# Optimization experiments

Hardware: AMD Instinct MI355X
Metric: run time of the kernel (lower is better)

Reference implementation:

```python
import jax, jax.numpy as jnp
import numpy as np

SEQ, EMB, OUT = 8192, 1024, 128

def setup_inputs() -> dict:
    key = jax.random.key(0)
    k1, k2, k3, k4 = jax.random.split(key, 4)
    return {
        "x": jax.random.normal(k1, (SEQ, EMB), dtype=jnp.float32),
        "wquery": jax.random.normal(k2, (EMB, OUT), dtype=jnp.float32) * (2.0 / EMB) ** 0.5,
        "wkey": jax.random.normal(k3, (EMB, OUT), dtype=jnp.float32) * (2.0 / EMB) ** 0.5,
        "wvalue": jax.random.normal(k4, (EMB, OUT), dtype=jnp.float32) * (2.0 / EMB) ** 0.5,
    }

def reference(x, wquery, wkey, wvalue):
    # Single-head attention, mask=True branch (mask tensor is zeros -> no masking).
    q = x @ wquery   # [S, D]
    k = x @ wkey     # [S, D]
    v = x @ wvalue   # [S, D]
    scale = jnp.sqrt(jnp.asarray(q.shape[-1], dtype=q.dtype))
    a = (q @ k.T) / scale              # [S, S]
    p = jax.nn.softmax(a, axis=1)      # softmax over keys (dim=1 in torch)
    return p @ v                       # [S, D]
```

## Files before the change

kernel.cpp:

```cpp
#include <hip/hip_runtime.h>
#include <cstdint>
#include <cstddef>

#define SEQ 8192
#define EMB 1024
#define DH  128

typedef __bf16 bf16x8 __attribute__((ext_vector_type(8)));
typedef __bf16 bf16x2 __attribute__((ext_vector_type(2)));
typedef float  f32x4  __attribute__((ext_vector_type(4)));
typedef float  f32x16 __attribute__((ext_vector_type(16)));
typedef uint32_t u32x4 __attribute__((ext_vector_type(4)));
typedef unsigned short u16x8 __attribute__((ext_vector_type(8)));

static constexpr float QSCALE = (float)(1.4426950408889634 / 11.313708498984760);

__device__ __forceinline__ unsigned short f2bf(float f) {
  uint32_t u = __builtin_bit_cast(uint32_t, f);
  u += 0x7FFFu + ((u >> 16) & 1u);
  return (unsigned short)(u >> 16);
}
__device__ __forceinline__ float bf2f(unsigned short u) {
  return __builtin_bit_cast(float, (uint32_t)u << 16);
}

#define GLD_LDS16(gsrc, ldst) \
  __builtin_amdgcn_global_load_lds((__attribute__((address_space(1))) void*)(gsrc), \
                                   (__attribute__((address_space(3))) void*)(ldst), 16, 0, 0)

__global__ __launch_bounds__(256) void convert_kernel(
    const float* __restrict__ wq, const float* __restrict__ wk, const float* __restrict__ wv,
    unsigned short* __restrict__ wt)
{
  const int bid = blockIdx.x;
  const int t = threadIdx.x;
  const int which = bid >> 2;
  const int k = (bid & 3) * 256 + t;
  const float* w = (which == 0) ? wq : ((which == 1) ? wk : wv);
  const float scl = (which == 0) ? QSCALE : 1.0f;
#pragma unroll
  for (int n = 0; n < 128; n += 4) {
    float4 v = *reinterpret_cast<const float4*>(w + (size_t)k * DH + n);
    wt[((size_t)which * DH + n + 0) * EMB + k] = f2bf(v.x * scl);
    wt[((size_t)which * DH + n + 1) * EMB + k] = f2bf(v.y * scl);
    wt[((size_t)which * DH + n + 2) * EMB + k] = f2bf(v.z * scl);
    wt[((size_t)which * DH + n + 3) * EMB + k] = f2bf(v.w * scl);
  }
}

__global__ __launch_bounds__(256) void qkv_gemm(
    const float* __restrict__ x, const unsigned short* __restrict__ wt,
    unsigned short* __restrict__ qs, unsigned short* __restrict__ ks,
    unsigned short* __restrict__ vt)
{
  __shared__ char LDS[49152];
  char* A0 = LDS;
  char* B0 = LDS + 16384;
  unsigned short* T = (unsigned short*)LDS;

  const int t    = threadIdx.x;
  const int lane = t & 63;
  const int wid  = t >> 6;
  const int wr   = wid >> 1, wc = wid & 1;
  const int l31  = lane & 31;
  const int hi   = lane >> 5;
  const int row0 = blockIdx.x * 64;
  const int which = blockIdx.y;

  const char* wtc = (const char*)(wt + (size_t)which * DH * EMB);

  const int arow = t >> 2;
  const int aq   = t & 3;
  const float* xrow = x + (size_t)(row0 + arow) * EMB + aq * 16;
  const int awz = (arow & 7) << 4;
  const int aoff0 = (aq * 32 + 0)  ^ awz;
  const int aoff1 = (aq * 32 + 16) ^ awz;

  f32x16 acc[2] = {};
  float4 xa0, xa1, xa2, xa3;

  auto ALOAD = [&](int k0) {
    const float* s = xrow + k0;
    xa0 = *reinterpret_cast<const float4*>(s + 0);
    xa1 = *reinterpret_cast<const float4*>(s + 4);
    xa2 = *reinterpret_cast<const float4*>(s + 8);
    xa3 = *reinterpret_cast<const float4*>(s + 12);
  };
  auto AWRITE = [&](int buf) {
    bf16x8 h0 = { (__bf16)xa0.x, (__bf16)xa0.y, (__bf16)xa0.z, (__bf16)xa0.w,
                  (__bf16)xa1.x, (__bf16)xa1.y, (__bf16)xa1.z, (__bf16)xa1.w };
    bf16x8 h1 = { (__bf16)xa2.x, (__bf16)xa2.y, (__bf16)xa2.z, (__bf16)xa2.w,
                  (__bf16)xa3.x, (__bf16)xa3.y, (__bf16)xa3.z, (__bf16)xa3.w };
    char* base = A0 + buf * 8192 + arow * 128;
    *reinterpret_cast<bf16x8*>(base + aoff0) = h0;
    *reinterpret_cast<bf16x8*>(base + aoff1) = h1;
  };
  auto BSTAGE = [&](int buf, int k0) {
#pragma unroll
    for (int i = 0; i < 4; ++i) {
      int bidx = i * 4096 + t * 16;
      int n = bidx >> 7, off = bidx & 127;
      const char* src = wtc + (size_t)n * (EMB * 2) + k0 * 2 + (off ^ ((n & 7) << 4));
      GLD_LDS16(src, B0 + buf * 16384 + i * 4096 + wid * 1024);
    }
  };

  constexpr int NI = EMB / 64;

  ALOAD(0);
  BSTAGE(0, 0);
  AWRITE(0);
  ALOAD(64);
  asm volatile("s_waitcnt vmcnt(4) lgkmcnt(0)" ::: "memory");
  __builtin_amdgcn_s_barrier();
  asm volatile("" ::: "memory");

  for (int it = 0; it < NI; ++it) {
    const int cur = it & 1;
    if (it + 1 < NI) BSTAGE(cur ^ 1, (it + 1) * 64);

    const char* Ab = A0 + cur * 8192;
    const char* Bb = B0 + cur * 16384;
    const int ar   = wr * 32 + l31;
    const int aswz = (l31 & 7) << 4;

    __builtin_amdgcn_s_setprio(1);
#pragma unroll
    for (int kk = 0; kk < 4; ++kk) {
      bf16x8 af = *reinterpret_cast<const bf16x8*>(Ab + ar * 128 + ((kk * 32 + hi * 16) ^ aswz));
#pragma unroll
      for (int nt = 0; nt < 2; ++nt) {
        const int n = wc * 64 + nt * 32 + l31;
        bf16x8 bf = *reinterpret_cast<const bf16x8*>(Bb + n * 128 + ((kk * 32 + hi * 16) ^ ((n & 7) << 4)));
        acc[nt] = __builtin_amdgcn_mfma_f32_32x32x16_bf16(af, bf, acc[nt], 0, 0, 0);
      }
    }
    __builtin_amdgcn_s_setprio(0);

    if (it + 1 < NI) {
      AWRITE(cur ^ 1);
      if (it + 2 < NI) {
        ALOAD((it + 2) * 64);
        asm volatile("s_waitcnt vmcnt(4) lgkmcnt(0)" ::: "memory");
      } else {
        asm volatile("s_waitcnt vmcnt(0) lgkmcnt(0)" ::: "memory");
      }
    }
    __builtin_amdgcn_s_barrier();
    asm volatile("" ::: "memory");
  }

  if (which < 2) {
    unsigned short* dst = (which == 0) ? qs : ks;
#pragma unroll
    for (int nt = 0; nt < 2; ++nt)
#pragma unroll
      for (int r = 0; r < 16; ++r) {
        int row = row0 + wr * 32 + (r & 3) + 8 * (r >> 2) + 4 * hi;
        dst[(size_t)row * DH + wc * 64 + nt * 32 + l31] = f2bf(acc[nt][r]);
      }
  } else {
    __syncthreads();
#pragma unroll
    for (int nt = 0; nt < 2; ++nt)
#pragma unroll
      for (int r = 0; r < 16; ++r) {
        int d  = wc * 64 + nt * 32 + l31;
        int rl = wr * 32 + (r & 3) + 8 * (r >> 2) + 4 * hi;
        T[d * 72 + rl] = f2bf(acc[nt][r]);
      }
    __syncthreads();
    const int d = t >> 1, half = t & 1;
#pragma unroll
    for (int i = 0; i < 4; ++i) {
      uint4 v = *reinterpret_cast<const uint4*>(&T[d * 72 + half * 32 + i * 8]);
      *reinterpret_cast<uint4*>(vt + (size_t)d * SEQ + row0 + half * 32 + i * 8) = v;
    }
  }
}

template <int NS>
__global__ __launch_bounds__(512, 2) void attn_kernel(
    const unsigned short* __restrict__ qs, const unsigned short* __restrict__ ks,
    const unsigned short* __restrict__ vt,
    unsigned short* __restrict__ Obf, float* __restrict__ ml)
{
  __shared__ unsigned short Ks[2][64 * 128];
  __shared__ unsigned short Vt[2][128 * 64];

  const int t    = threadIdx.x;
  const int lane = t & 63;
  const int wid  = t >> 6;
  const int l31  = lane & 31;
  const int hi   = lane >> 5;
  const int kswz = (l31 & 15) << 4;
  const int q0   = blockIdx.x * 256 + wid * 32;
  const int sp   = blockIdx.y;

  bf16x8 qf[8];
  {
    const unsigned short* qp = qs + (size_t)(q0 + l31) * DH + hi * 8;
#pragma unroll
    for (int ds = 0; ds < 8; ++ds)
      qf[ds] = *reinterpret_cast<const bf16x8*>(qp + ds * 16);
  }

  float l = 0.f;
  f32x16 O[4] = {};

  const char* ksc = (const char*)ks;
  const char* vtc = (const char*)vt;
  char* ksl = (char*)&Ks[0][0];
  char* vtl = (char*)&Vt[0][0];

  constexpr int CHUNK = SEQ / NS;
  constexpr int NT = CHUNK / 64;
  const int kv_base = sp * CHUNK;

  auto KSTAGE = [&](int tile) {
    const int kv0 = kv_base + tile * 64;
#pragma unroll
    for (int rr = 0; rr < 2; ++rr) {
      int bidx = rr * 512 + t;
      int key = bidx >> 4, blk = bidx & 15;
      const char* src = ksc + (size_t)(kv0 + key) * 256 + ((blk * 16) ^ ((key & 15) << 4));
      GLD_LDS16(src, ksl + (tile & 1) * 16384 + rr * 8192 + wid * 1024);
    }
  };
  auto VSTAGE = [&](int tile) {
    const int kv0 = kv_base + tile * 64;
#pragma unroll
    for (int rr = 0; rr < 2; ++rr) {
      int bidx = rr * 512 + t;
      int rowi = bidx >> 4, ci = bidx & 15;
      int s = ci ^ (rowi & 15);
      int d = rowi * 2 + (s >> 3);
      int kb = s & 7;
      const char* src = vtc + (size_t)d * (SEQ * 2) + (size_t)kv0 * 2 + kb * 16;
      GLD_LDS16(src, vtl + (tile & 1) * 16384 + rr * 8192 + wid * 1024);
    }
  };

  auto QKT = [&](f32x16& T0, f32x16& T1, int tile) {
    const char* kb = ksl + (tile & 1) * 16384;
    f32x16 z = {};
    T0 = z; T1 = z;
#pragma unroll
    for (int ds = 0; ds < 8; ++ds) {
      bf16x8 ka = *reinterpret_cast<const bf16x8*>(kb + l31 * 256 + ((ds * 32 + hi * 16) ^ kswz));
      T0 = __builtin_amdgcn_mfma_f32_32x32x16_bf16(ka, qf[ds], T0, 0, 0, 0);
    }
#pragma unroll
    for (int ds = 0; ds < 8; ++ds) {
      bf16x8 ka = *reinterpret_cast<const bf16x8*>(kb + 8192 + l31 * 256 + ((ds * 32 + hi * 16) ^ kswz));
      T1 = __builtin_amdgcn_mfma_f32_32x32x16_bf16(ka, qf[ds], T1, 0, 0, 0);
    }
  };

  auto build2 = [&](const f32x16& P, bf16x8* fr) {
    uint32_t c[8];
#pragma unroll
    for (int i = 0; i < 8; ++i) {
      bf16x2 b2; b2[0] = (__bf16)P[2 * i]; b2[1] = (__bf16)P[2 * i + 1];
      c[i] = __builtin_bit_cast(uint32_t, b2);
    }
    uint32_t r0 = __shfl_xor(c[0], 32, 64), r1 = __shfl_xor(c[1], 32, 64);
    uint32_t r2 = __shfl_xor(c[2], 32, 64), r3 = __shfl_xor(c[3], 32, 64);
    u32x4 w0;
    w0[0] = hi ? r2 : c[0];
    w0[1] = hi ? r3 : c[1];
    w0[2] = hi ? c[2] : r0;
    w0[3] = hi ? c[3] : r1;
    uint32_t r4 = __shfl_xor(c[4], 32, 64), r5 = __shfl_xor(c[5], 32, 64);
    uint32_t r6 = __shfl_xor(c[6], 32, 64), r7 = __shfl_xor(c[7], 32, 64);
    u32x4 w1;
    w1[0] = hi ? r6 : c[4];
    w1[1] = hi ? r7 : c[5];
    w1[2] = hi ? c[6] : r4;
    w1[3] = hi ? c[7] : r5;
    fr[0] = __builtin_bit_cast(bf16x8, w0);
    fr[1] = __builtin_bit_cast(bf16x8, w1);
  };

  auto BODY = [&](int it, f32x16& Sc0, f32x16& Sc1, f32x16& Sn0, f32x16& Sn1) {
    if (it + 2 < NT) KSTAGE(it + 2);
    if (it + 1 < NT) VSTAGE(it + 1);

    if (it + 1 < NT) {
      __builtin_amdgcn_s_setprio(1);
      QKT(Sn0, Sn1, it + 1);
      __builtin_amdgcn_s_setprio(0);
    }

    float sm[16];
#pragma unroll
    for (int r = 0; r < 16; ++r) {
      Sc0[r] = __builtin_amdgcn_exp2f(Sc0[r]);
      Sc1[r] = __builtin_amdgcn_exp2f(Sc1[r]);
      sm[r] = Sc0[r] + Sc1[r];
    }
#pragma unroll
    for (int st = 8; st >= 1; st >>= 1)
#pragma unroll
      for (int r = 0; r < st; ++r) sm[r] += sm[r + st];
    l += sm[0] + __shfl_xor(sm[0], 32, 64);

    bf16x8 pa[4];
    build2(Sc0, &pa[0]);
    build2(Sc1, &pa[2]);

    const char* vb0 = vtl + (it & 1) * 16384;
    __builtin_amdgcn_s_setprio(1);
#pragma unroll
    for (int ks4 = 0; ks4 < 4; ++ks4) {
#pragma unroll
      for (int nt = 0; nt < 4; ++nt) {
        const int d = nt * 32 + l31;
        const int vrow = d >> 1;
        const int within = (((d & 1) << 3) | (ks4 * 2 + hi)) ^ (vrow & 15);
        bf16x8 vb = *reinterpret_cast<const bf16x8*>(vb0 + vrow * 256 + within * 16);
        O[nt] = __builtin_amdgcn_mfma_f32_32x32x16_bf16(pa[ks4], vb, O[nt], 0, 0, 0);
      }
    }
    __builtin_amdgcn_s_setprio(0);

    asm volatile("s_waitcnt vmcnt(0)" ::: "memory");
    __builtin_amdgcn_s_barrier();
    asm volatile("" ::: "memory");
  };

  KSTAGE(0); VSTAGE(0); KSTAGE(1);
  asm volatile("s_waitcnt vmcnt(0)" ::: "memory");
  __builtin_amdgcn_s_barrier();
  asm volatile("" ::: "memory");

  f32x16 Sa0, Sa1, Sb0, Sb1;
  QKT(Sa0, Sa1, 0);
  asm volatile("" ::: "memory");
  __builtin_amdgcn_s_barrier();
  asm volatile("" ::: "memory");

  for (int it = 0; it < NT; it += 2) {
    BODY(it,     Sa0, Sa1, Sb0, Sb1);
    BODY(it + 1, Sb0, Sb1, Sa0, Sa1);
  }

  const float linv = 1.0f / l;
  unsigned short* Obase = Obf + ((size_t)sp * SEQ + q0) * DH;
#pragma unroll
  for (int r = 0; r < 16; ++r) {
    const int row = (r & 3) + 8 * (r >> 2) + 4 * hi;
    const float li = __shfl(linv, row, 64);
#pragma unroll
    for (int nt = 0; nt < 4; ++nt)
      Obase[(size_t)row * DH + nt * 32 + l31] = f2bf(O[nt][r] * li);
  }
  if (lane < 32) {
    ml[(size_t)sp * (2 * SEQ) + q0 + lane]       = 0.0f;
    ml[(size_t)sp * (2 * SEQ) + SEQ + q0 + lane] = l;
  }
}

template <int NS>
__global__ __launch_bounds__(256) void combine_kernel(
    const unsigned short* __restrict__ Obf, const float* __restrict__ ml, float* __restrict__ out)
{
  const int idx = blockIdx.x * 256 + threadIdx.x;
  const int s = idx >> 4;
  const int c = (idx & 15) * 8;
  float mv[NS], lv[NS];
  float M = -__builtin_inff();
#pragma unroll
  for (int i = 0; i < NS; ++i) {
    mv[i] = ml[(size_t)i * (2 * SEQ) + s];
    lv[i] = ml[(size_t)i * (2 * SEQ) + SEQ + s];
    M = fmaxf(M, mv[i]);
  }
  float den = 0.f;
  float num[8] = {};
#pragma unroll
  for (int i = 0; i < NS; ++i) {
    float g = __builtin_amdgcn_exp2f(mv[i] - M) * lv[i];
    den += g;
    u16x8 o = *reinterpret_cast<const u16x8*>(&Obf[((size_t)i * SEQ + s) * DH + c]);
#pragma unroll
    for (int j = 0; j < 8; ++j) num[j] += g * bf2f(o[j]);
  }
  const float inv = 1.f / den;
  f32x4 r0, r1;
#pragma unroll
  for (int j = 0; j < 4; ++j) { r0[j] = num[j] * inv; r1[j] = num[j + 4] * inv; }
  *reinterpret_cast<f32x4*>(&out[(size_t)s * DH + c])     = r0;
  *reinterpret_cast<f32x4*>(&out[(size_t)s * DH + c + 4]) = r1;
}

extern "C" void kernel_launch(void* const* d_in, const int* in_sizes, int n_in,
                              void* d_out, int out_size, void* d_ws, size_t ws_size,
                              hipStream_t stream) {
  const float* x  = (const float*)d_in[0];
  const float* wq = (const float*)d_in[1];
  const float* wk = (const float*)d_in[2];
  const float* wv = (const float*)d_in[3];
  float* out = (float*)d_out;

  char* ws = (char*)d_ws;
  const size_t MB = 1024 * 1024;
  unsigned short* qs = (unsigned short*)(ws);
  unsigned short* ks = (unsigned short*)(ws + 2 * MB);
  unsigned short* vt = (unsigned short*)(ws + 4 * MB);
  unsigned short* wt = (unsigned short*)(ws + 6 * MB);

  convert_kernel<<<12, 256, 0, stream>>>(wq, wk, wv, wt);
  qkv_gemm<<<dim3(SEQ / 64, 3), 256, 0, stream>>>(x, wt, qs, ks, vt);

  unsigned short* Obf = (unsigned short*)(ws + 6 * MB);
  const size_t need8 = 6 * MB + 8ull * SEQ * DH * 2 + 8ull * 2 * SEQ * 4;
  if (ws_size >= need8) {
    float* ml = (float*)(ws + 6 * MB + 8ull * SEQ * DH * 2);
    attn_kernel<8><<<dim3(SEQ / 256, 8), 512, 0, stream>>>(qs, ks, vt, Obf, ml);
    combine_kernel<8><<<SEQ * DH / 8 / 256, 256, 0, stream>>>(Obf, ml, out);
  } else {
    float* ml = (float*)(ws + 6 * MB + 4ull * SEQ * DH * 2);
    attn_kernel<4><<<dim3(SEQ / 256, 4), 512, 0, stream>>>(qs, ks, vt, Obf, ml);
    combine_kernel<4><<<SEQ * DH / 8 / 256, 256, 0, stream>>>(Obf, ml, out);
  }
}
```

Before: 78.29 us.

## Double QKV GEMM block to 512 threads with one 32x32 tile per wave

The QKV projection GEMM now runs 8 waves per block instead of 4, so each wave computes a single 32x32 MFMA tile rather than two. The LDS layout of A and B changes to a paired-row XOR swizzle so that each thread stages one 16-byte chunk per load. The aim is more waves in flight to hide global-load latency in this memory-heavy stage. The cost is fewer MFMAs per barrier and more synchronisation per unit of work.

```diff
diff --git a/kernel.cpp b/kernel.cpp
--- a/kernel.cpp
+++ b/kernel.cpp
@@ -48,7 +48,7 @@
   }
 }
 
-__global__ __launch_bounds__(256) void qkv_gemm(
+__global__ __launch_bounds__(512) void qkv_gemm(
     const float* __restrict__ x, const unsigned short* __restrict__ wt,
     unsigned short* __restrict__ qs, unsigned short* __restrict__ ks,
     unsigned short* __restrict__ vt)
@@ -61,7 +61,8 @@
   const int t    = threadIdx.x;
   const int lane = t & 63;
   const int wid  = t >> 6;
-  const int wr   = wid >> 1, wc = wid & 1;
+  const int wr   = wid >> 2;
+  const int wc   = wid & 3;
   const int l31  = lane & 31;
   const int hi   = lane >> 5;
   const int row0 = blockIdx.x * 64;
@@ -69,39 +70,34 @@
 
   const char* wtc = (const char*)(wt + (size_t)which * DH * EMB);
 
-  const int arow = t >> 2;
-  const int aq   = t & 3;
-  const float* xrow = x + (size_t)(row0 + arow) * EMB + aq * 16;
-  const int awz = (arow & 7) << 4;
-  const int aoff0 = (aq * 32 + 0)  ^ awz;
-  const int aoff1 = (aq * 32 + 16) ^ awz;
-
-  f32x16 acc[2] = {};
-  float4 xa0, xa1, xa2, xa3;
+  const int arow = t >> 3;
+  const int ac8  = t & 7;
+  const float* xrow = x + (size_t)(row0 + arow) * EMB + ac8 * 8;
+  const int awoff = (arow >> 1) * 256 + ((((arow & 1) << 3) | ac8) ^ ((arow >> 1) & 15)) * 16;
+
+  f32x16 acc = {};
+  float4 xa0, xa1;
 
   auto ALOAD = [&](int k0) {
     const float* s = xrow + k0;
     xa0 = *reinterpret_cast<const float4*>(s + 0);
     xa1 = *reinterpret_cast<const float4*>(s + 4);
-    xa2 = *reinterpret_cast<const float4*>(s + 8);
-    xa3 = *reinterpret_cast<const float4*>(s + 12);
   };
   auto AWRITE = [&](int buf) {
-    bf16x8 h0 = { (__bf16)xa0.x, (__bf16)xa0.y, (__bf16)xa0.z, (__bf16)xa0.w,
-                  (__bf16)xa1.x, (__bf16)xa1.y, (__bf16)xa1.z, (__bf16)xa1.w };
-    bf16x8 h1 = { (__bf16)xa2.x, (__bf16)xa2.y, (__bf16)xa2.z, (__bf16)xa2.w,
-                  (__bf16)xa3.x, (__bf16)xa3.y, (__bf16)xa3.z, (__bf16)xa3.w };
-    char* base = A0 + buf * 8192 + arow * 128;
-    *reinterpret_cast<bf16x8*>(base + aoff0) = h0;
-    *reinterpret_cast<bf16x8*>(base + aoff1) = h1;
+    bf16x8 h = { (__bf16)xa0.x, (__bf16)xa0.y, (__bf16)xa0.z, (__bf16)xa0.w,
+                 (__bf16)xa1.x, (__bf16)xa1.y, (__bf16)xa1.z, (__bf16)xa1.w };
+    *reinterpret_cast<bf16x8*>(A0 + buf * 8192 + awoff) = h;
   };
   auto BSTAGE = [&](int buf, int k0) {
 #pragma unroll
-    for (int i = 0; i < 4; ++i) {
-      int bidx = i * 4096 + t * 16;
-      int n = bidx >> 7, off = bidx & 127;
-      const char* src = wtc + (size_t)n * (EMB * 2) + k0 * 2 + (off ^ ((n & 7) << 4));
-      GLD_LDS16(src, B0 + buf * 16384 + i * 4096 + wid * 1024);
+    for (int rr = 0; rr < 2; ++rr) {
+      int bidx = rr * 512 + t;
+      int rowi = bidx >> 4, ci = bidx & 15;
+      int s = ci ^ (rowi & 15);
+      int n = rowi * 2 + (s >> 3);
+      int kc = s & 7;
+      const char* src = wtc + (size_t)n * (EMB * 2) + k0 * 2 + kc * 16;
+      GLD_LDS16(src, B0 + buf * 16384 + rr * 8192 + wid * 1024);
     }
   };
 
@@ -111,9 +107,18 @@
   BSTAGE(0, 0);
   AWRITE(0);
   ALOAD(64);
-  asm volatile("s_waitcnt vmcnt(4) lgkmcnt(0)" ::: "memory");
+  asm volatile("s_waitcnt vmcnt(2) lgkmcnt(0)" ::: "memory");
   __builtin_amdgcn_s_barrier();
   asm volatile("" ::: "memory");
+
+  const int ar   = wr * 32 + l31;
+  const int apr  = ar >> 1;
+  const int asel = (ar & 1) << 3;
+  const int axr  = apr & 15;
+  const int bn   = wc * 32 + l31;
+  const int bpr  = bn >> 1;
+  const int bsel = (bn & 1) << 3;
+  const int bxr  = bpr & 15;
 
   for (int it = 0; it < NI; ++it) {
     const int cur = it & 1;
@@ -121,19 +126,14 @@
 
     const char* Ab = A0 + cur * 8192;
     const char* Bb = B0 + cur * 16384;
-    const int ar   = wr * 32 + l31;
-    const int aswz = (l31 & 7) << 4;
 
     __builtin_amdgcn_s_setprio(1);
 #pragma unroll
     for (int kk = 0; kk < 4; ++kk) {
-      bf16x8 af = *reinterpret_cast<const bf16x8*>(Ab + ar * 128 + ((kk * 32 + hi * 16) ^ aswz));
-#pragma unroll
-      for (int nt = 0; nt < 2; ++nt) {
-        const int n = wc * 64 + nt * 32 + l31;
-        bf16x8 bf = *reinterpret_cast<const bf16x8*>(Bb + n * 128 + ((kk * 32 + hi * 16) ^ ((n & 7) << 4)));
-        acc[nt] = __builtin_amdgcn_mfma_f32_32x32x16_bf16(af, bf, acc[nt], 0, 0, 0);
-      }
+      const int c = kk * 2 + hi;
+      bf16x8 af = *reinterpret_cast<const bf16x8*>(Ab + apr * 256 + ((asel | c) ^ axr) * 16);
+      bf16x8 bf = *reinterpret_cast<const bf16x8*>(Bb + bpr * 256 + ((bsel | c) ^ bxr) * 16);
+      acc = __builtin_amdgcn_mfma_f32_32x32x16_bf16(af, bf, acc, 0, 0, 0);
     }
     __builtin_amdgcn_s_setprio(0);
 
@@ -141,7 +141,7 @@
       AWRITE(cur ^ 1);
       if (it + 2 < NI) {
         ALOAD((it + 2) * 64);
-        asm volatile("s_waitcnt vmcnt(4) lgkmcnt(0)" ::: "memory");
+        asm volatile("s_waitcnt vmcnt(2) lgkmcnt(0)" ::: "memory");
       } else {
         asm volatile("s_waitcnt vmcnt(0) lgkmcnt(0)" ::: "memory");
       }
@@ -153,28 +153,25 @@
   if (which < 2) {
     unsigned short* dst = (which == 0) ? qs : ks;
 #pragma unroll
-    for (int nt = 0; nt < 2; ++nt)
-#pragma unroll
-      for (int r = 0; r < 16; ++r) {
-        int row = row0 + wr * 32 + (r & 3) + 8 * (r >> 2) + 4 * hi;
-        dst[(size_t)row * DH + wc * 64 + nt * 32 + l31] = f2bf(acc[nt][r]);
-      }
+    for (int r = 0; r < 16; ++r) {
+      int row = row0 + wr * 32 + (r & 3) + 8 * (r >> 2) + 4 * hi;
+      dst[(size_t)row * DH + wc * 32 + l31] = f2bf(acc[r]);
+    }
   } else {
     __syncthreads();
 #pragma unroll
-    for (int nt = 0; nt < 2; ++nt)
-#pragma unroll
-      for (int r = 0; r < 16; ++r) {
-        int d  = wc * 64 + nt * 32 + l31;
-        int rl = wr * 32 + (r & 3) + 8 * (r >> 2) + 4 * hi;
-        T[d * 72 + rl] = f2bf(acc[nt][r]);
-      }
+    for (int r = 0; r < 16; ++r) {
+      int d  = wc * 32 + l31;
+      int rl = wr * 32 + (r & 3) + 8 * (r >> 2) + 4 * hi;
+      T[d * 72 + rl] = f2bf(acc[r]);
+    }
     __syncthreads();
-    const int d = t >> 1, half = t & 1;
-#pragma unroll
-    for (int i = 0; i < 4; ++i) {
-      uint4 v = *reinterpret_cast<const uint4*>(&T[d * 72 + half * 32 + i * 8]);
-      *reinterpret_cast<uint4*>(vt + (size_t)d * SEQ + row0 + half * 32 + i * 8) = v;
+    const int d = t >> 2;
+    const int c0 = (t & 3) * 16;
+#pragma unroll
+    for (int i = 0; i < 2; ++i) {
+      uint4 v = *reinterpret_cast<const uint4*>(&T[d * 72 + c0 + i * 8]);
+      *reinterpret_cast<uint4*>(vt + (size_t)d * SEQ + row0 + c0 + i * 8) = v;
     }
   }
 }
@@ -411,7 +408,7 @@
   unsigned short* wt = (unsigned short*)(ws + 6 * MB);
 
   convert_kernel<<<12, 256, 0, stream>>>(wq, wk, wv, wt);
-  qkv_gemm<<<dim3(SEQ / 64, 3), 256, 0, stream>>>(x, wt, qs, ks, vt);
+  qkv_gemm<<<dim3(SEQ / 64, 3), 512, 0, stream>>>(x, wt, qs, ks, vt);
 
   unsigned short* Obf = (unsigned short*)(ws + 6 * MB);
   const size_t need8 = 6 * MB + 8ull * SEQ * DH * 2 + 8ull * 2 * SEQ * 4;
```

New measurement: 75.50 us. 1.04x faster.
